# Kernel tuning notes

Measured on AMD Instinct MI355X. Metric: run time of the kernel, lower is better.

## Reference

```python
import jax, jax.numpy as jnp
import numpy as np

D_MODEL = 1024
H = 16
DK = D_MODEL // H
D_FC = 4096
B = 2
S = 1024
EPS = 1e-6


def setup_inputs() -> dict:
    key = jax.random.key(0)
    ks = jax.random.split(key, 8)
    sc = 1.0 / np.sqrt(D_MODEL)
    return {
        "x": jax.random.normal(ks[0], (B, S, D_MODEL), dtype=jnp.float32),
        "mask": jnp.ones((B, 1, 1, S), dtype=jnp.int32),
        "w_q": jax.random.normal(ks[1], (D_MODEL, D_MODEL), dtype=jnp.float32) * sc,
        "w_k": jax.random.normal(ks[2], (D_MODEL, D_MODEL), dtype=jnp.float32) * sc,
        "w_v": jax.random.normal(ks[3], (D_MODEL, D_MODEL), dtype=jnp.float32) * sc,
        "w_o": jax.random.normal(ks[4], (D_MODEL, D_MODEL), dtype=jnp.float32) * sc,
        "alpha1": jnp.ones((D_MODEL,), dtype=jnp.float32),
        "beta1": jnp.zeros((D_MODEL,), dtype=jnp.float32),
        "alpha2": jnp.ones((D_MODEL,), dtype=jnp.float32),
        "beta2": jnp.zeros((D_MODEL,), dtype=jnp.float32),
        "fc1_w": jax.random.normal(ks[5], (D_FC, D_MODEL), dtype=jnp.float32) * sc,
        "fc1_b": jnp.zeros((D_FC,), dtype=jnp.float32),
        "fc2_w": jax.random.normal(ks[6], (D_MODEL, D_FC), dtype=jnp.float32) * (1.0 / np.sqrt(D_FC)),
        "fc2_b": jnp.zeros((D_MODEL,), dtype=jnp.float32),
    }


def _layernorm(x, alpha, beta):
    # Matches torch: mean and std (unbiased, ddof=1), divide by (std + eps)
    mean = jnp.mean(x, axis=-1, keepdims=True)
    std = jnp.std(x, axis=-1, keepdims=True, ddof=1)
    return alpha * (x - mean) / (std + EPS) + beta


def _mha(x, mask, w_q, w_k, w_v, w_o):
    # nn.Linear(bias=False): y = x @ W.T
    q = (x @ w_q.T).reshape(B, S, H, DK).transpose(0, 2, 1, 3)  # (B,H,S,DK)
    k = (x @ w_k.T).reshape(B, S, H, DK).transpose(0, 2, 1, 3)
    v = (x @ w_v.T).reshape(B, S, H, DK).transpose(0, 2, 1, 3)
    scores = jnp.einsum('bhqd,bhkd->bhqk', q, k) / jnp.sqrt(jnp.float32(DK))
    scores = jnp.where(mask == 0, jnp.float32(-1e9), scores)
    attn = jax.nn.softmax(scores, axis=-1)  # dropout=0 (eval)
    out = jnp.einsum('bhqk,bhkd->bhqd', attn, v)  # (B,H,S,DK)
    out = out.transpose(0, 2, 1, 3).reshape(B, S, D_MODEL)
    return out @ w_o.T


def _ffn(x, fc1_w, fc1_b, fc2_w, fc2_b):
    h = jax.nn.relu(x @ fc1_w.T + fc1_b)
    return h @ fc2_w.T + fc2_b


def reference(x, mask, w_q, w_k, w_v, w_o, alpha1, beta1, alpha2, beta2,
              fc1_w, fc1_b, fc2_w, fc2_b):
    # Pre-LN residual block 1: attention
    x = x + _mha(_layernorm(x, alpha1, beta1), mask, w_q, w_k, w_v, w_o)
    # Pre-LN residual block 2: FFN
    x = x + _ffn(_layernorm(x, alpha2, beta2), fc1_w, fc1_b, fc2_w, fc2_b)
    return x
```

## Files before the change

### kernel.cpp

```cpp
#include <hip/hip_runtime.h>
#include <hip/hip_bf16.h>


typedef __bf16 bf16;
typedef __attribute__((ext_vector_type(8))) __bf16 bf16x8;
typedef __attribute__((ext_vector_type(4))) __bf16 bf16x4;
typedef __attribute__((ext_vector_type(4))) float f32x4;
typedef __attribute__((ext_vector_type(16))) float f32x16;
typedef __attribute__((ext_vector_type(4))) unsigned int u32x4;

#define NTOK 2048
#define DM   1024
#define DFC  4096
#define QKVN 3072

__device__ inline void gl_lds16(const void* g, void* l) {
    __builtin_amdgcn_global_load_lds((const __attribute__((address_space(1))) void*)g,
                                     (__attribute__((address_space(3))) void*)l, 16, 0, 0);
}

__device__ inline unsigned cvtpk_bf16(float lo, float hi) {
    unsigned r;
    asm("v_cvt_pk_bf16_f32 %0, %1, %2" : "=v"(r) : "v"(lo), "v"(hi));
    return r;
}

__device__ inline void ln_row(float4 v, const float* alpha, const float* beta,
                              bf16* outrow, int t) {
    float s  = v.x + v.y + v.z + v.w;
    float ss = v.x * v.x + v.y * v.y + v.z * v.z + v.w * v.w;
    __shared__ float red[8];
    int lane = t & 63, wv = t >> 6;
    #pragma unroll
    for (int o = 32; o > 0; o >>= 1) {
        s  += __shfl_down(s, o);
        ss += __shfl_down(ss, o);
    }
    if (lane == 0) { red[wv] = s; red[4 + wv] = ss; }
    __syncthreads();
    float S  = red[0] + red[1] + red[2] + red[3];
    float SS = red[4] + red[5] + red[6] + red[7];
    float mean = S * (1.0f / 1024.0f);
    float var  = (SS - S * mean) * (1.0f / 1023.0f);
    var = var < 0.f ? 0.f : var;
    float inv = 1.0f / (sqrtf(var) + 1e-6f);
    float4 a4 = reinterpret_cast<const float4*>(alpha)[t];
    float4 b4 = reinterpret_cast<const float4*>(beta)[t];
    bf16x4 o4;
    o4[0] = (bf16)(a4.x * (v.x - mean) * inv + b4.x);
    o4[1] = (bf16)(a4.y * (v.y - mean) * inv + b4.y);
    o4[2] = (bf16)(a4.z * (v.z - mean) * inv + b4.z);
    o4[3] = (bf16)(a4.w * (v.w - mean) * inv + b4.w);
    reinterpret_cast<bf16x4*>(outrow)[t] = o4;
}

__global__ __launch_bounds__(256) void prep_kernel(
    const float4* __restrict__ wq, const float4* __restrict__ wk,
    const float4* __restrict__ wv, bf16x4* __restrict__ oqkv,
    const float* __restrict__ x, const float* __restrict__ alpha1,
    const float* __restrict__ beta1, bf16* __restrict__ xn) {
    int blk = blockIdx.x;
    int t = threadIdx.x;
    if (blk < 3072) {
        int i = blk * 256 + t;
        const int Q = 262144;
        float4 v = (i < Q) ? wq[i] : (i < 2 * Q) ? wk[i - Q] : wv[i - 2 * Q];
        bf16x4 o;
        o[0] = (bf16)v.x; o[1] = (bf16)v.y; o[2] = (bf16)v.z; o[3] = (bf16)v.w;
        oqkv[i] = o;
    } else {
        int row = blk - 3072;
        float4 v = reinterpret_cast<const float4*>(x + (size_t)row * DM)[t];
        ln_row(v, alpha1, beta1, xn + (size_t)row * DM, t);
    }
}

__global__ __launch_bounds__(256) void reduce_ln_kernel(const float* __restrict__ p,
                                                        const float* __restrict__ resid,
                                                        const float* __restrict__ alpha,
                                                        const float* __restrict__ beta,
                                                        float* __restrict__ x2,
                                                        bf16* __restrict__ xn) {
    int row = blockIdx.x, t = threadIdx.x;
    size_t i4 = (size_t)row * 256 + t;
    const size_t SL = 524288;
    float4 a = reinterpret_cast<const float4*>(p)[i4];
    float4 b = reinterpret_cast<const float4*>(p)[i4 + SL];
    float4 c = reinterpret_cast<const float4*>(p)[i4 + 2 * SL];
    float4 d = reinterpret_cast<const float4*>(p)[i4 + 3 * SL];
    float4 r = reinterpret_cast<const float4*>(resid)[i4];
    float4 v;
    v.x = a.x + b.x + c.x + d.x + r.x;
    v.y = a.y + b.y + c.y + d.y + r.y;
    v.z = a.z + b.z + c.z + d.z + r.z;
    v.w = a.w + b.w + c.w + d.w + r.w;
    reinterpret_cast<float4*>(x2)[i4] = v;
    ln_row(v, alpha, beta, xn + (size_t)row * DM, t);
}

__global__ __launch_bounds__(256) void reduce_out_kernel(const float* __restrict__ p,
                                                         const float* __restrict__ bias,
                                                         const float* __restrict__ x2,
                                                         float* __restrict__ out) {
    size_t i4 = (size_t)blockIdx.x * 256 + threadIdx.x;
    const size_t SL = 524288;
    float4 a = reinterpret_cast<const float4*>(p)[i4];
    float4 b = reinterpret_cast<const float4*>(p)[i4 + SL];
    float4 c = reinterpret_cast<const float4*>(p)[i4 + 2 * SL];
    float4 d = reinterpret_cast<const float4*>(p)[i4 + 3 * SL];
    float4 r = reinterpret_cast<const float4*>(x2)[i4];
    float4 bi = reinterpret_cast<const float4*>(bias)[i4 & 255];
    float4 o;
    o.x = a.x + b.x + c.x + d.x + r.x + bi.x;
    o.y = a.y + b.y + c.y + d.y + r.y + bi.y;
    o.z = a.z + b.z + c.z + d.z + r.z + bi.z;
    o.w = a.w + b.w + c.w + d.w + r.w + bi.w;
    reinterpret_cast<float4*>(out)[i4] = o;
}

template <int EPI>
__global__ __launch_bounds__(256) void gemm128(const bf16* __restrict__ A,
                                               const bf16* __restrict__ Bt,
                                               void* __restrict__ outp,
                                               bf16* __restrict__ vt,
                                               int M, int N, int K, int kslice,
                                               int nbx, int nby) {
    __shared__ bf16 As[2][128 * 64];
    __shared__ bf16 Bs[2][128 * 64];
    int tid = threadIdx.x;
    int lane = tid & 63, wave = tid >> 6;
    int q = lane >> 4, r = lane & 15;
    int wm = wave >> 1, wn = wave & 1;

    int lid = blockIdx.y * nbx + blockIdx.x;
    int nxp = nbx >> 3;
    int xcd = lid & 7;
    int loc = lid >> 3;
    int bx = xcd * nxp + (loc % nxp);
    int by = loc / nxp;

    int m0 = by * 128, n0 = bx * 128;
    int kbeg = blockIdx.z * kslice;
    int nit = kslice / 64;
    f32x4 acc[4][4] = {};

    int srow = tid >> 3;
    int csrc = (tid & 7) ^ (srow & 7);
    const bf16* agp = A  + (size_t)(m0 + srow) * K + kbeg + csrc * 8;
    const bf16* bgp = Bt + (size_t)(n0 + srow) * K + kbeg + csrc * 8;

    int co0 = ((q ^ (r & 7)) * 8);
    int co1 = co0 ^ 32;
    int aoff = (wm * 64 + r) * 64;
    int boff = (wn * 64 + r) * 64;

    auto stage = [&](int it, int b) {
        int k0 = it * 64;
        #pragma unroll
        for (int j = 0; j < 4; ++j) {
            gl_lds16(agp + (size_t)j * 32 * K + k0, &As[b][tid * 8 + j * 2048]);
            gl_lds16(bgp + (size_t)j * 32 * K + k0, &Bs[b][tid * 8 + j * 2048]);
        }
    };

    stage(0, 0);
    for (int it = 0; it < nit; ++it) {
        __syncthreads();
        if (it + 1 < nit) stage(it + 1, (it + 1) & 1);
        const bf16* Ab = &As[it & 1][aoff];
        const bf16* Bb = &Bs[it & 1][boff];
        #pragma unroll
        for (int half = 0; half < 2; ++half) {
            int co = half ? co1 : co0;
            bf16x8 af[4], bfv[4];
            #pragma unroll
            for (int t = 0; t < 4; ++t)
                af[t] = *reinterpret_cast<const bf16x8*>(Ab + t * 1024 + co);
            #pragma unroll
            for (int u = 0; u < 4; ++u)
                bfv[u] = *reinterpret_cast<const bf16x8*>(Bb + u * 1024 + co);
            #pragma unroll
            for (int t = 0; t < 4; ++t)
                #pragma unroll
                for (int u = 0; u < 4; ++u)
                    acc[t][u] = __builtin_amdgcn_mfma_f32_16x16x32_bf16(af[t], bfv[u], acc[t][u], 0, 0, 0);
        }
    }

    if (EPI == 2 && n0 >= 2048) {
        int bb = m0 >> 10;
        int sb = (m0 & 1023) + wm * 64 + q * 4;
        int vrow0 = bb * 1024 + (n0 - 2048) + wn * 64;
        #pragma unroll
        for (int t = 0; t < 4; ++t) {
            #pragma unroll
            for (int u = 0; u < 4; ++u) {
                bf16x4 pk;
                #pragma unroll
                for (int i = 0; i < 4; ++i) pk[i] = (bf16)acc[t][u][i];
                *reinterpret_cast<bf16x4*>(vt + (size_t)(vrow0 + u * 16 + r) * 1024 + sb + t * 16) = pk;
            }
        }
        return;
    }

    size_t zoff = (size_t)blockIdx.z * M * N;
    #pragma unroll
    for (int t = 0; t < 4; ++t) {
        #pragma unroll
        for (int u = 0; u < 4; ++u) {
            #pragma unroll
            for (int i = 0; i < 4; ++i) {
                int mm = m0 + wm * 64 + t * 16 + q * 4 + i;
                int nn = n0 + wn * 64 + u * 16 + r;
                size_t idx = (size_t)mm * N + nn;
                float v = acc[t][u][i];
                if (EPI == 2) {
                    ((bf16*)outp)[idx] = (bf16)v;
                } else {
                    ((float*)outp)[zoff + idx] = v;
                }
            }
        }
    }
}

template <int EPI>
__global__ __launch_bounds__(512) void gemm_3buf(const bf16* __restrict__ A,
                                                 const bf16* __restrict__ Bt,
                                                 void* __restrict__ outp,
                                                 const float* __restrict__ bias,
                                                 int M, int N, int K, int kslice,
                                                 int nbx, int nby) {
    __shared__ bf16 As[3][128 * 64];
    __shared__ bf16 Bs[3][256 * 64];
    int tid = threadIdx.x;
    int lane = tid & 63, wave = tid >> 6;
    int q = lane >> 4, r = lane & 15;
    int wm = wave >> 2, wn = wave & 3;

    int bx, by;
    if (nbx >= 8) {
        int lid = blockIdx.y * nbx + blockIdx.x;
        int nxp = nbx >> 3;
        int xcd = lid & 7;
        int loc = lid >> 3;
        bx = xcd * nxp + (loc % nxp);
        by = loc / nxp;
    } else {
        bx = blockIdx.x; by = blockIdx.y;
    }

    int m0 = by * 128, n0 = bx * 256;
    int kbeg = blockIdx.z * kslice;
    int nt = kslice / 64;
    f32x4 acc[4][4] = {};

    int srow = tid >> 3;
    int csrc = (tid & 7) ^ (srow & 7);
    const bf16* agp = A  + (size_t)(m0 + srow) * K + kbeg + csrc * 8;
    const bf16* bgp = Bt + (size_t)(n0 + srow) * K + kbeg + csrc * 8;

    int co0 = ((q ^ (r & 7)) * 8);
    int aoff = (wm * 64 + r) * 64;
    int boff = (wn * 64 + r) * 64;

    auto stage_p0 = [&](int it, int b) {
        int k0 = it * 64;
        gl_lds16(agp + k0,                  &As[b][tid * 8]);
        gl_lds16(agp + (size_t)64 * K + k0, &As[b][4096 + tid * 8]);
        gl_lds16(bgp + k0,                  &Bs[b][tid * 8]);
    };
    auto stage_p1 = [&](int it, int b) {
        int k0 = it * 64;
        gl_lds16(bgp + (size_t)64 * K + k0,  &Bs[b][4096 + tid * 8]);
        gl_lds16(bgp + (size_t)128 * K + k0, &Bs[b][8192 + tid * 8]);
        gl_lds16(bgp + (size_t)192 * K + k0, &Bs[b][12288 + tid * 8]);
    };

    stage_p0(0, 0); stage_p1(0, 0);
    stage_p0(1, 1); stage_p1(1, 1);
    asm volatile("s_waitcnt vmcnt(6)" ::: "memory");
    __builtin_amdgcn_s_barrier();

    for (int t = 0; t < nt; ++t) {
        const bf16* Ab = &As[t % 3][aoff];
        const bf16* Bb = &Bs[t % 3][boff];
        bool pf = (t + 2) < nt;
        int nb = (t + 2) % 3;
        #pragma unroll
        for (int ph = 0; ph < 2; ++ph) {
            int co = co0 ^ (ph * 32);
            bf16x8 af[4], bfv[4];
            #pragma unroll
            for (int tt = 0; tt < 4; ++tt)
                af[tt] = *reinterpret_cast<const bf16x8*>(Ab + tt * 1024 + co);
            #pragma unroll
            for (int u = 0; u < 4; ++u)
                bfv[u] = *reinterpret_cast<const bf16x8*>(Bb + u * 1024 + co);
            if (pf) {
                if (ph == 0) stage_p0(t + 2, nb);
                else         stage_p1(t + 2, nb);
            }
            __builtin_amdgcn_s_setprio(1);
            #pragma unroll
            for (int tt = 0; tt < 4; ++tt)
                #pragma unroll
                for (int u = 0; u < 4; ++u)
                    acc[tt][u] = __builtin_amdgcn_mfma_f32_16x16x32_bf16(
                        af[tt], bfv[u], acc[tt][u], 0, 0, 0);
            __builtin_amdgcn_s_setprio(0);
        }
        if (t + 1 < nt) {
            if (pf) asm volatile("s_waitcnt vmcnt(6)" ::: "memory");
            else    asm volatile("s_waitcnt vmcnt(0)" ::: "memory");
            __builtin_amdgcn_s_barrier();
        }
    }

    size_t zoff = (size_t)blockIdx.z * M * N;
    #pragma unroll
    for (int tt = 0; tt < 4; ++tt) {
        #pragma unroll
        for (int u = 0; u < 4; ++u) {
            #pragma unroll
            for (int i = 0; i < 4; ++i) {
                int mm = m0 + wm * 64 + tt * 16 + q * 4 + i;
                int nn = n0 + wn * 64 + u * 16 + r;
                size_t idx = (size_t)mm * N + nn;
                float v = acc[tt][u][i];
                if (EPI == 1) {
                    v += bias[nn];
                    ((bf16*)outp)[idx] = (bf16)(v > 0.f ? v : 0.f);
                } else {
                    ((float*)outp)[zoff + idx] = v;
                }
            }
        }
    }
}

__global__ __launch_bounds__(256) void attn_kernel(const bf16* __restrict__ qkv,
                                                   const bf16* __restrict__ Vt,
                                                   const int* __restrict__ mask,
                                                   bf16* __restrict__ out,
                                                   const float4* __restrict__ cwo,
                                                   const float4* __restrict__ cf1,
                                                   const float4* __restrict__ cf2,
                                                   bf16x4* __restrict__ oo,
                                                   bf16x4* __restrict__ of1,
                                                   bf16x4* __restrict__ of2) {
    __shared__ bf16 Ks[2][4096];
    __shared__ bf16 Vs[2][4096];
    __shared__ float msk[1024];
    __shared__ float als[4][32];
    int tid = threadIdx.x;

    if (blockIdx.x >= 256) {
        int base = (blockIdx.x - 256) * 1024;
        const int Q = 262144;
        #pragma unroll
        for (int k = 0; k < 4; ++k) {
            int i = base + k * 256 + tid;
            float4 v;
            bf16x4* dst;
            if (i < Q)          { v = cwo[i];         dst = oo  + i; }
            else if (i < 5 * Q) { v = cf1[i - Q];     dst = of1 + (i - Q); }
            else                { v = cf2[i - 5 * Q]; dst = of2 + (i - 5 * Q); }
            bf16x4 o;
            o[0] = (bf16)v.x; o[1] = (bf16)v.y; o[2] = (bf16)v.z; o[3] = (bf16)v.w;
            *dst = o;
        }
        return;
    }

    int lane = tid & 63, w = tid >> 6;
    int l5 = lane & 31, hi = lane >> 5;

    int id = blockIdx.x;
    int xcd = id & 7, jj = id >> 3;
    int bh = xcd * 4 + (jj >> 3);
    int qb = jj & 7;
    int b = bh >> 4, h = bh & 15;

    {
        int4 mi = reinterpret_cast<const int4*>(mask + b * 1024)[tid];
        msk[tid * 4 + 0] = mi.x ? 0.f : -1e9f;
        msk[tid * 4 + 1] = mi.y ? 0.f : -1e9f;
        msk[tid * 4 + 2] = mi.z ? 0.f : -1e9f;
        msk[tid * 4 + 3] = mi.w ? 0.f : -1e9f;
    }

    int qrow0 = qb * 128 + w * 32;
    const bf16* qp = qkv + (size_t)(b * 1024 + qrow0 + l5) * QKVN + h * 64 + hi * 8;
    bf16x8 qf[4];
    #pragma unroll
    for (int ks = 0; ks < 4; ++ks)
        qf[ks] = *reinterpret_cast<const bf16x8*>(qp + ks * 16);

    int csw = (tid & 7) ^ ((tid >> 3) & 7);
    const bf16* kg0 = qkv + (size_t)(b * 1024 + (tid >> 3)) * QKVN + 1024 + h * 64 + csw * 8;
    const bf16* kg1 = kg0 + (size_t)32 * QKVN;
    const bf16* vg0 = Vt + (size_t)((b * 16 + h) * 64 + (tid >> 3)) * 1024 + csw * 8;
    const bf16* vg1 = vg0 + 32 * 1024;
    bf16* kld = &Ks[0][tid * 8];
    bf16* vld = &Vs[0][tid * 8];

    gl_lds16(kg0, kld);
    gl_lds16(kg1, kld + 2048);
    gl_lds16(vg0, vld);
    gl_lds16(vg1, vld + 2048);

    float m_run = -1e30f, l_half = 0.f;
    f32x16 o0 = {};
    f32x16 o1 = {};

    for (int t = 0; t < 16; ++t) {
        __syncthreads();
        if (t < 15) {
            int ktn = (t + 1) * 64;
            int bo = ((t + 1) & 1) * 4096;
            gl_lds16(kg0 + (size_t)ktn * QKVN, kld + bo);
            gl_lds16(kg1 + (size_t)ktn * QKVN, kld + bo + 2048);
            gl_lds16(vg0 + ktn, vld + bo);
            gl_lds16(vg1 + ktn, vld + bo + 2048);
        }
        const bf16* Kb = Ks[t & 1];
        const bf16* Vb = Vs[t & 1];
        int kt = t * 64;

        f32x16 s0 = {}, s1 = {};
        __builtin_amdgcn_s_setprio(1);
        #pragma unroll
        for (int ks = 0; ks < 4; ++ks) {
            int ch = (((ks << 1) + hi) ^ (l5 & 7)) << 3;
            bf16x8 k0 = *reinterpret_cast<const bf16x8*>(&Kb[l5 * 64 + ch]);
            bf16x8 k1 = *reinterpret_cast<const bf16x8*>(&Kb[(32 + l5) * 64 + ch]);
            s0 = __builtin_amdgcn_mfma_f32_32x32x16_bf16(k0, qf[ks], s0, 0, 0, 0);
            s1 = __builtin_amdgcn_mfma_f32_32x32x16_bf16(k1, qf[ks], s1, 0, 0, 0);
        }
        __builtin_amdgcn_s_setprio(0);

        float p0[16], p1[16];
        float pmax = -1e30f;
        #pragma unroll
        for (int g = 0; g < 4; ++g) {
            float4 mb0 = *reinterpret_cast<const float4*>(&msk[kt + g * 8 + hi * 4]);
            float4 mb1 = *reinterpret_cast<const float4*>(&msk[kt + 32 + g * 8 + hi * 4]);
            #pragma unroll
            for (int i = 0; i < 4; ++i) {
                float mbv0 = (i == 0) ? mb0.x : (i == 1) ? mb0.y : (i == 2) ? mb0.z : mb0.w;
                float mbv1 = (i == 0) ? mb1.x : (i == 1) ? mb1.y : (i == 2) ? mb1.z : mb1.w;
                float a0 = fmaf(s0[g * 4 + i], 0.125f, mbv0);
                float a1 = fmaf(s1[g * 4 + i], 0.125f, mbv1);
                p0[g * 4 + i] = a0;
                p1[g * 4 + i] = a1;
                pmax = fmaxf(pmax, fmaxf(a0, a1));
            }
        }
        pmax = fmaxf(pmax, __shfl_xor(pmax, 32));
        float mnew = fmaxf(m_run, pmax);
        if (!__all(pmax - m_run <= 8.0f)) {
            float alpha = __expf(m_run - mnew);
            m_run = mnew;
            l_half *= alpha;
            als[w][l5] = alpha;
            #pragma unroll
            for (int g = 0; g < 4; ++g) {
                float4 av = *reinterpret_cast<const float4*>(&als[w][g * 8 + hi * 4]);
                o0[g * 4 + 0] *= av.x; o0[g * 4 + 1] *= av.y;
                o0[g * 4 + 2] *= av.z; o0[g * 4 + 3] *= av.w;
                o1[g * 4 + 0] *= av.x; o1[g * 4 + 1] *= av.y;
                o1[g * 4 + 2] *= av.z; o1[g * 4 + 3] *= av.w;
            }
        }
        float sum = 0.f;
        #pragma unroll
        for (int rg = 0; rg < 16; ++rg) {
            p0[rg] = __expf(p0[rg] - m_run);
            p1[rg] = __expf(p1[rg] - m_run);
            sum += p0[rg] + p1[rg];
        }
        l_half += sum;

        __builtin_amdgcn_s_setprio(1);
        #pragma unroll
        for (int tile = 0; tile < 2; ++tile) {
            const float* pp = tile ? p1 : p0;
            #pragma unroll
            for (int kp = 0; kp < 2; ++kp) {
                unsigned uA0 = cvtpk_bf16(pp[8 * kp + 0], pp[8 * kp + 1]);
                unsigned uA1 = cvtpk_bf16(pp[8 * kp + 2], pp[8 * kp + 3]);
                unsigned uB0 = cvtpk_bf16(pp[8 * kp + 4], pp[8 * kp + 5]);
                unsigned uB1 = cvtpk_bf16(pp[8 * kp + 6], pp[8 * kp + 7]);
                unsigned us0 = hi ? uB0 : uA0, us1 = hi ? uB1 : uA1;
                unsigned ug0 = hi ? uA0 : uB0, ug1 = hi ? uA1 : uB1;
                unsigned r0 = (unsigned)__shfl_xor((int)ug0, 32);
                unsigned r1 = (unsigned)__shfl_xor((int)ug1, 32);
                u32x4 pw_;
                pw_[0] = hi ? r0 : us0;
                pw_[1] = hi ? r1 : us1;
                pw_[2] = hi ? us0 : r0;
                pw_[3] = hi ? us1 : r1;
                bf16x8 pf = *reinterpret_cast<bf16x8*>(&pw_);
                int vch = (((tile << 2) + (kp << 1) + hi) ^ (l5 & 7)) << 3;
                bf16x8 v0 = *reinterpret_cast<const bf16x8*>(&Vb[l5 * 64 + vch]);
                bf16x8 v1 = *reinterpret_cast<const bf16x8*>(&Vb[(32 + l5) * 64 + vch]);
                o0 = __builtin_amdgcn_mfma_f32_32x32x16_bf16(pf, v0, o0, 0, 0, 0);
                o1 = __builtin_amdgcn_mfma_f32_32x32x16_bf16(pf, v1, o1, 0, 0, 0);
            }
        }
        __builtin_amdgcn_s_setprio(0);
    }

    float l_tot = l_half + __shfl_xor(l_half, 32);
    als[w][l5] = 1.0f / l_tot;
    bf16* ob = out + (size_t)(b * 1024 + qrow0) * DM + h * 64;
    #pragma unroll
    for (int g = 0; g < 4; ++g) {
        float4 iv = *reinterpret_cast<const float4*>(&als[w][g * 8 + hi * 4]);
        #pragma unroll
        for (int i = 0; i < 4; ++i) {
            float ivv = (i == 0) ? iv.x : (i == 1) ? iv.y : (i == 2) ? iv.z : iv.w;
            int qr = g * 8 + hi * 4 + i;
            ob[(size_t)qr * DM + l5]      = (bf16)(o0[g * 4 + i] * ivv);
            ob[(size_t)qr * DM + 32 + l5] = (bf16)(o1[g * 4 + i] * ivv);
        }
    }
}

extern "C" void kernel_launch(void* const* d_in, const int* in_sizes, int n_in,
                              void* d_out, int out_size, void* d_ws, size_t ws_size,
                              hipStream_t stream) {
    const float* x      = (const float*)d_in[0];
    const int*   mask   = (const int*)  d_in[1];
    const float* w_q    = (const float*)d_in[2];
    const float* w_k    = (const float*)d_in[3];
    const float* w_v    = (const float*)d_in[4];
    const float* w_o    = (const float*)d_in[5];
    const float* alpha1 = (const float*)d_in[6];
    const float* beta1  = (const float*)d_in[7];
    const float* alpha2 = (const float*)d_in[8];
    const float* beta2  = (const float*)d_in[9];
    const float* fc1_w  = (const float*)d_in[10];
    const float* fc1_b  = (const float*)d_in[11];
    const float* fc2_w  = (const float*)d_in[12];
    const float* fc2_b  = (const float*)d_in[13];
    float* out = (float*)d_out;

    char* ws = (char*)d_ws;
    const size_t MB = 1024 * 1024;
    bf16*  wqkv_b = (bf16*)(ws +  0 * MB);
    bf16*  wo_b   = (bf16*)(ws +  6 * MB);
    bf16*  f1w_b  = (bf16*)(ws +  8 * MB);
    bf16*  f2w_b  = (bf16*)(ws + 16 * MB);
    bf16*  xn     = (bf16*)(ws + 24 * MB);
    bf16*  qkvb   = (bf16*)(ws + 28 * MB);
    bf16*  vtb    = (bf16*)(ws + 40 * MB);
    bf16*  attnb  = (bf16*)(ws + 44 * MB);
    float* x2     = (float*)(ws + 48 * MB);
    float* po     = (float*)(ws + 56 * MB);
    bf16*  hb     = (bf16*)(ws + 28 * MB);
    float* pf2    = (float*)(ws + 56 * MB);

    prep_kernel<<<5120, 256, 0, stream>>>(
        (const float4*)w_q, (const float4*)w_k, (const float4*)w_v,
        (bf16x4*)wqkv_b, x, alpha1, beta1, xn);

    gemm128<2><<<dim3(24, 16, 1), 256, 0, stream>>>(
        xn, wqkv_b, qkvb, vtb, NTOK, QKVN, DM, DM, 24, 16);

    attn_kernel<<<2560, 256, 0, stream>>>(
        qkvb, vtb, mask, attnb,
        (const float4*)w_o, (const float4*)fc1_w, (const float4*)fc2_w,
        (bf16x4*)wo_b, (bf16x4*)f1w_b, (bf16x4*)f2w_b);

    gemm128<4><<<dim3(8, 16, 4), 256, 0, stream>>>(
        attnb, wo_b, po, nullptr, NTOK, DM, DM, DM / 4, 8, 16);

    reduce_ln_kernel<<<NTOK, 256, 0, stream>>>(po, x, alpha2, beta2, x2, xn);

    gemm_3buf<1><<<dim3(16, 16, 1), 512, 0, stream>>>(
        xn, f1w_b, hb, fc1_b, NTOK, DFC, DM, DM, 16, 16);

    gemm_3buf<4><<<dim3(4, 16, 4), 512, 0, stream>>>(
        hb, f2w_b, pf2, nullptr, NTOK, DM, DFC, DFC / 4, 4, 16);

    reduce_out_kernel<<<2048, 256, 0, stream>>>(pf2, fc2_b, x2, out);
}
```

Baseline: 236.7 us.

## Halve attention block size to 64 query rows with 2 warps for more blocks

Attention blocks now use 128 threads (2 wavefronts) and cover 64 query rows instead of 128, so the grid doubles to 512 attention blocks. This aims to fill the GPU's many CUs better, since 256 blocks underfill the device. The K/V tile staging is rewritten to load each 64-key tile with 4 chunks per thread, and the weight-conversion tail blocks process 8 float4 per thread. In exchange, every K/V tile is loaded from global memory twice as often across blocks, and fewer waves per block are available to hide latency.

```diff
diff --git a/kernel.cpp b/kernel.cpp
--- a/kernel.cpp
+++ b/kernel.cpp
@@ -340,7 +340,7 @@
     }
 }
 
-__global__ __launch_bounds__(256) void attn_kernel(const bf16* __restrict__ qkv,
+__global__ __launch_bounds__(128) void attn_kernel(const bf16* __restrict__ qkv,
                                                    const bf16* __restrict__ Vt,
                                                    const int* __restrict__ mask,
                                                    bf16* __restrict__ out,
@@ -353,15 +353,15 @@
     __shared__ bf16 Ks[2][4096];
     __shared__ bf16 Vs[2][4096];
     __shared__ float msk[1024];
-    __shared__ float als[4][32];
+    __shared__ float als[2][32];
     int tid = threadIdx.x;
 
-    if (blockIdx.x >= 256) {
-        int base = (blockIdx.x - 256) * 1024;
+    if (blockIdx.x >= 512) {
+        int base = (blockIdx.x - 512) * 1024;
         const int Q = 262144;
         #pragma unroll
-        for (int k = 0; k < 4; ++k) {
-            int i = base + k * 256 + tid;
+        for (int k = 0; k < 8; ++k) {
+            int i = base + k * 128 + tid;
             float4 v;
             bf16x4* dst;
             if (i < Q)          { v = cwo[i];         dst = oo  + i; }
@@ -379,19 +379,21 @@
 
     int id = blockIdx.x;
     int xcd = id & 7, jj = id >> 3;
-    int bh = xcd * 4 + (jj >> 3);
-    int qb = jj & 7;
+    int bh = xcd * 4 + (jj >> 4);
+    int qb = jj & 15;
     int b = bh >> 4, h = bh & 15;
 
-    {
-        int4 mi = reinterpret_cast<const int4*>(mask + b * 1024)[tid];
-        msk[tid * 4 + 0] = mi.x ? 0.f : -1e9f;
-        msk[tid * 4 + 1] = mi.y ? 0.f : -1e9f;
-        msk[tid * 4 + 2] = mi.z ? 0.f : -1e9f;
-        msk[tid * 4 + 3] = mi.w ? 0.f : -1e9f;
-    }
-
-    int qrow0 = qb * 128 + w * 32;
+    #pragma unroll
+    for (int j = 0; j < 2; ++j) {
+        int mi4 = tid + j * 128;
+        int4 mi = reinterpret_cast<const int4*>(mask + b * 1024)[mi4];
+        msk[mi4 * 4 + 0] = mi.x ? 0.f : -1e9f;
+        msk[mi4 * 4 + 1] = mi.y ? 0.f : -1e9f;
+        msk[mi4 * 4 + 2] = mi.z ? 0.f : -1e9f;
+        msk[mi4 * 4 + 3] = mi.w ? 0.f : -1e9f;
+    }
+
+    int qrow0 = qb * 64 + w * 32;
     const bf16* qp = qkv + (size_t)(b * 1024 + qrow0 + l5) * QKVN + h * 64 + hi * 8;
     bf16x8 qf[4];
     #pragma unroll
@@ -399,17 +401,22 @@
         qf[ks] = *reinterpret_cast<const bf16x8*>(qp + ks * 16);
 
     int csw = (tid & 7) ^ ((tid >> 3) & 7);
-    const bf16* kg0 = qkv + (size_t)(b * 1024 + (tid >> 3)) * QKVN + 1024 + h * 64 + csw * 8;
-    const bf16* kg1 = kg0 + (size_t)32 * QKVN;
-    const bf16* vg0 = Vt + (size_t)((b * 16 + h) * 64 + (tid >> 3)) * 1024 + csw * 8;
-    const bf16* vg1 = vg0 + 32 * 1024;
+    const bf16* kgb = qkv + (size_t)(b * 1024 + (tid >> 3)) * QKVN + 1024 + h * 64 + csw * 8;
+    const bf16* vgb = Vt + (size_t)((b * 16 + h) * 64 + (tid >> 3)) * 1024 + csw * 8;
     bf16* kld = &Ks[0][tid * 8];
     bf16* vld = &Vs[0][tid * 8];
 
-    gl_lds16(kg0, kld);
-    gl_lds16(kg1, kld + 2048);
-    gl_lds16(vg0, vld);
-    gl_lds16(vg1, vld + 2048);
+    auto stage_tile = [&](int t, int bo) {
+        int ktn = t * 64;
+        #pragma unroll
+        for (int c = 0; c < 4; ++c) {
+            gl_lds16(kgb + (size_t)(ktn + c * 16) * QKVN, kld + bo + c * 1024);
+            gl_lds16(vgb + (size_t)(c * 16) * 1024 + ktn,  vld + bo + c * 1024);
+        }
+    };
+
+    int co_dummy = 0; (void)co_dummy;
+    stage_tile(0, 0);
 
     float m_run = -1e30f, l_half = 0.f;
     f32x16 o0 = {};
@@ -417,14 +424,7 @@
 
     for (int t = 0; t < 16; ++t) {
         __syncthreads();
-        if (t < 15) {
-            int ktn = (t + 1) * 64;
-            int bo = ((t + 1) & 1) * 4096;
-            gl_lds16(kg0 + (size_t)ktn * QKVN, kld + bo);
-            gl_lds16(kg1 + (size_t)ktn * QKVN, kld + bo + 2048);
-            gl_lds16(vg0 + ktn, vld + bo);
-            gl_lds16(vg1 + ktn, vld + bo + 2048);
-        }
+        if (t < 15) stage_tile(t + 1, ((t + 1) & 1) * 4096);
         const bf16* Kb = Ks[t & 1];
         const bf16* Vb = Vs[t & 1];
         int kt = t * 64;
@@ -570,7 +570,7 @@
     gemm128<2><<<dim3(24, 16, 1), 256, 0, stream>>>(
         xn, wqkv_b, qkvb, vtb, NTOK, QKVN, DM, DM, 24, 16);
 
-    attn_kernel<<<2560, 256, 0, stream>>>(
+    attn_kernel<<<2816, 128, 0, stream>>>(
         qkvb, vtb, mask, attnb,
         (const float4*)w_o, (const float4*)fc1_w, (const float4*)fc2_w,
         (bf16x4*)wo_b, (bf16x4*)f1w_b, (bf16x4*)f2w_b);
```

Result: slower. 243.2 us (+2.8%).

## Split attention KV range in two with separate combine kernel

Applied to the files above, without the earlier changes.

Each attention block now handles half of the key/value sequence, which doubles the number of attention blocks from 256 to 512 and should fill more CUs. Every block writes its unnormalized fp32 output plus per-row running max and sum to workspace. A new combine kernel merges the two halves with a log-sum-exp rescale and writes the bf16 attention output. The cost is an extra kernel launch, extra fp32 traffic to global memory, and the combine pass itself.

```diff
diff --git a/kernel.cpp b/kernel.cpp
--- a/kernel.cpp
+++ b/kernel.cpp
@@ -118,6 +118,32 @@
     reinterpret_cast<float4*>(out)[i4] = o;
 }
 
+__global__ __launch_bounds__(256) void combine_kernel(const float* __restrict__ oraw,
+                                                      const float2* __restrict__ ml,
+                                                      bf16* __restrict__ attnb) {
+    int s = blockIdx.x;
+    int t = threadIdx.x;
+    int b = s >> 10;
+    int h = t >> 4;
+    int bh = b * 16 + h;
+    int sr = s & 1023;
+    float2 ml0 = ml[bh * 1024 + sr];
+    float2 ml1 = ml[32768 + bh * 1024 + sr];
+    float M  = fmaxf(ml0.x, ml1.x);
+    float w0 = __expf(ml0.x - M);
+    float w1 = __expf(ml1.x - M);
+    float inv = 1.0f / (w0 * ml0.y + w1 * ml1.y);
+    size_t i4 = (size_t)s * 256 + t;
+    float4 a = reinterpret_cast<const float4*>(oraw)[i4];
+    float4 c = reinterpret_cast<const float4*>(oraw + (size_t)2048 * 1024)[i4];
+    bf16x4 o;
+    o[0] = (bf16)((w0 * a.x + w1 * c.x) * inv);
+    o[1] = (bf16)((w0 * a.y + w1 * c.y) * inv);
+    o[2] = (bf16)((w0 * a.z + w1 * c.z) * inv);
+    o[3] = (bf16)((w0 * a.w + w1 * c.w) * inv);
+    reinterpret_cast<bf16x4*>(attnb)[i4] = o;
+}
+
 template <int EPI>
 __global__ __launch_bounds__(256) void gemm128(const bf16* __restrict__ A,
                                                const bf16* __restrict__ Bt,
@@ -343,7 +369,8 @@
 __global__ __launch_bounds__(256) void attn_kernel(const bf16* __restrict__ qkv,
                                                    const bf16* __restrict__ Vt,
                                                    const int* __restrict__ mask,
-                                                   bf16* __restrict__ out,
+                                                   float* __restrict__ oraw,
+                                                   float2* __restrict__ mlbuf,
                                                    const float4* __restrict__ cwo,
                                                    const float4* __restrict__ cf1,
                                                    const float4* __restrict__ cf2,
@@ -356,8 +383,8 @@
     __shared__ float als[4][32];
     int tid = threadIdx.x;
 
-    if (blockIdx.x >= 256) {
-        int base = (blockIdx.x - 256) * 1024;
+    if (blockIdx.x >= 512) {
+        int base = (blockIdx.x - 512) * 1024;
         const int Q = 262144;
         #pragma unroll
         for (int k = 0; k < 4; ++k) {
@@ -379,8 +406,10 @@
 
     int id = blockIdx.x;
     int xcd = id & 7, jj = id >> 3;
-    int bh = xcd * 4 + (jj >> 3);
-    int qb = jj & 7;
+    int bh = xcd * 4 + (jj >> 4);
+    int rest = jj & 15;
+    int qb  = rest >> 1;
+    int kvh = rest & 1;
     int b = bh >> 4, h = bh & 15;
 
     {
@@ -406,28 +435,31 @@
     bf16* kld = &Ks[0][tid * 8];
     bf16* vld = &Vs[0][tid * 8];
 
-    gl_lds16(kg0, kld);
-    gl_lds16(kg1, kld + 2048);
-    gl_lds16(vg0, vld);
-    gl_lds16(vg1, vld + 2048);
+    {
+        int ktn = kvh * 512;
+        gl_lds16(kg0 + (size_t)ktn * QKVN, kld);
+        gl_lds16(kg1 + (size_t)ktn * QKVN, kld + 2048);
+        gl_lds16(vg0 + ktn, vld);
+        gl_lds16(vg1 + ktn, vld + 2048);
+    }
 
     float m_run = -1e30f, l_half = 0.f;
     f32x16 o0 = {};
     f32x16 o1 = {};
 
-    for (int t = 0; t < 16; ++t) {
+    for (int tt = 0; tt < 8; ++tt) {
         __syncthreads();
-        if (t < 15) {
-            int ktn = (t + 1) * 64;
-            int bo = ((t + 1) & 1) * 4096;
+        if (tt < 7) {
+            int ktn = (kvh * 8 + tt + 1) * 64;
+            int bo = ((tt + 1) & 1) * 4096;
             gl_lds16(kg0 + (size_t)ktn * QKVN, kld + bo);
             gl_lds16(kg1 + (size_t)ktn * QKVN, kld + bo + 2048);
             gl_lds16(vg0 + ktn, vld + bo);
             gl_lds16(vg1 + ktn, vld + bo + 2048);
         }
-        const bf16* Kb = Ks[t & 1];
-        const bf16* Vb = Vs[t & 1];
-        int kt = t * 64;
+        const bf16* Kb = Ks[tt & 1];
+        const bf16* Vb = Vs[tt & 1];
+        int kt = (kvh * 8 + tt) * 64;
 
         f32x16 s0 = {}, s1 = {};
         __builtin_amdgcn_s_setprio(1);
@@ -514,18 +546,20 @@
     }
 
     float l_tot = l_half + __shfl_xor(l_half, 32);
-    als[w][l5] = 1.0f / l_tot;
-    bf16* ob = out + (size_t)(b * 1024 + qrow0) * DM + h * 64;
+    float* orow = oraw + (size_t)kvh * (2048u * 1024u)
+                + (size_t)(b * 1024 + qrow0) * 1024 + h * 64;
     #pragma unroll
     for (int g = 0; g < 4; ++g) {
-        float4 iv = *reinterpret_cast<const float4*>(&als[w][g * 8 + hi * 4]);
         #pragma unroll
         for (int i = 0; i < 4; ++i) {
-            float ivv = (i == 0) ? iv.x : (i == 1) ? iv.y : (i == 2) ? iv.z : iv.w;
             int qr = g * 8 + hi * 4 + i;
-            ob[(size_t)qr * DM + l5]      = (bf16)(o0[g * 4 + i] * ivv);
-            ob[(size_t)qr * DM + 32 + l5] = (bf16)(o1[g * 4 + i] * ivv);
-        }
+            orow[(size_t)qr * 1024 + l5]      = o0[g * 4 + i];
+            orow[(size_t)qr * 1024 + 32 + l5] = o1[g * 4 + i];
+        }
+    }
+    if (hi == 0) {
+        float2 v; v.x = m_run; v.y = l_tot;
+        mlbuf[kvh * 32768 + bh * 1024 + qrow0 + l5] = v;
     }
 }
 
@@ -559,6 +593,8 @@
     bf16*  vtb    = (bf16*)(ws + 40 * MB);
     bf16*  attnb  = (bf16*)(ws + 44 * MB);
     float* x2     = (float*)(ws + 48 * MB);
+    float* oraw   = (float*)(ws + 56 * MB);
+    float2* mlbuf = (float2*)(ws + 72 * MB);
     float* po     = (float*)(ws + 56 * MB);
     bf16*  hb     = (bf16*)(ws + 28 * MB);
     float* pf2    = (float*)(ws + 56 * MB);
@@ -570,11 +606,13 @@
     gemm128<2><<<dim3(24, 16, 1), 256, 0, stream>>>(
         xn, wqkv_b, qkvb, vtb, NTOK, QKVN, DM, DM, 24, 16);
 
-    attn_kernel<<<2560, 256, 0, stream>>>(
-        qkvb, vtb, mask, attnb,
+    attn_kernel<<<2816, 256, 0, stream>>>(
+        qkvb, vtb, mask, oraw, mlbuf,
         (const float4*)w_o, (const float4*)fc1_w, (const float4*)fc2_w,
         (bf16x4*)wo_b, (bf16x4*)f1w_b, (bf16x4*)f2w_b);
 
+    combine_kernel<<<2048, 256, 0, stream>>>(oraw, mlbuf, attnb);
+
     gemm128<4><<<dim3(8, 16, 4), 256, 0, stream>>>(
         attnb, wo_b, po, nullptr, NTOK, DM, DM, DM / 4, 8, 16);
 
```

Measured after the change: 245.4 us. +3.7%, slower.
